# Kernel optimization log

Measured on AMD Instinct MI355X. Metric: run time of the kernel, lower is better.

Reference implementation:

```python
import jax, jax.numpy as jnp
import numpy as np

D_IN, D_OUT = 128, 128


def setup_inputs() -> dict:
    key = jax.random.key(0)
    ks = jax.random.split(key, 12)
    B = 262144
    g = 1.0 / np.sqrt(D_IN)
    gc = 1.0 / np.sqrt(D_IN + D_OUT)
    go = 1.0 / np.sqrt(D_OUT)
    return {
        "x": jax.random.normal(ks[0], (B, D_IN), jnp.float32),
        "h_prev": jax.random.normal(ks[1], (1, D_OUT), jnp.float32) * 0.1,
        "W_slow_w": jax.random.normal(ks[2], (D_OUT, D_IN), jnp.float32) * g,
        "W_slow_b": jnp.zeros((D_OUT,), jnp.float32),
        "W_fast_w": jnp.zeros((D_OUT, D_IN), jnp.float32),
        "Wi_w": jax.random.normal(ks[3], (D_OUT, D_IN), jnp.float32) * g,
        "Wi_b": jnp.zeros((D_OUT,), jnp.float32),
        "Wf_w": jax.random.normal(ks[4], (D_OUT, D_IN + D_OUT), jnp.float32) * gc,
        "Wf_b": jnp.zeros((D_OUT,), jnp.float32),
        "Wo_w": jax.random.normal(ks[5], (D_OUT, D_OUT), jnp.float32) * go,
        "Wo_b": jnp.zeros((D_OUT,), jnp.float32),
        "ln_g": jnp.ones((D_OUT,), jnp.float32),
        "ln_b": jnp.zeros((D_OUT,), jnp.float32),
    }


def _linear(x, w, b=None):
    y = x @ w.T
    return y if b is None else y + b


def _layernorm(x, g, b, eps=1e-5):
    mu = jnp.mean(x, axis=-1, keepdims=True)
    var = jnp.var(x, axis=-1, keepdims=True)
    return (x - mu) * jax.lax.rsqrt(var + eps) * g + b


def reference(x, h_prev, W_slow_w, W_slow_b, W_fast_w, Wi_w, Wi_b,
              Wf_w, Wf_b, Wo_w, Wo_b, ln_g, ln_b):
    B = x.shape[0]
    hp = jnp.broadcast_to(h_prev, (B, h_prev.shape[1]))  # [B, d_out]
    i_t = jax.nn.sigmoid(_linear(x, Wi_w, Wi_b))
    f_t = jax.nn.sigmoid(_linear(jnp.concatenate([x, hp], axis=1), Wf_w, Wf_b))
    h_slow = _linear(x, W_slow_w, W_slow_b)
    h_fast = _linear(x, W_fast_w)
    h_raw = i_t * (h_slow + h_fast) + f_t * hp
    o_t = jax.nn.sigmoid(_linear(h_raw, Wo_w, Wo_b))
    h_out = o_t * jnp.tanh(h_raw)
    return _layernorm(h_out, ln_g, ln_b)
```

## Files before the change

kernel.cpp:

```cpp
#include <hip/hip_runtime.h>
#include <hip/hip_bf16.h>
#include <hip/hip_fp16.h>


typedef __attribute__((ext_vector_type(8)))  short short8;
typedef __attribute__((ext_vector_type(16))) float f32x16;

__device__ __forceinline__ unsigned short f2bf(float f) {
    union { float f; unsigned u; } v; v.f = f;
    unsigned r = v.u + 0x7fffu + ((v.u >> 16) & 1u);
    return (unsigned short)(r >> 16);
}
__device__ __forceinline__ float bf2f(unsigned hs) {
    union { unsigned u; float f; } v; v.u = hs << 16;
    return v.f;
}
__device__ __forceinline__ unsigned pk_bf16(float lo, float hi) {
    union { __hip_bfloat162 h; unsigned u; } c;
    c.h = __float22bfloat162_rn(make_float2(lo, hi));
    return c.u;
}
__device__ __forceinline__ unsigned pk_f16(float lo, float hi) {
    union { __half2 h; unsigned u; } c;
    c.h = __floats2half2_rn(lo, hi);
    return c.u;
}
__device__ __forceinline__ float lo_f16(unsigned u) {
    union { unsigned u; __half2 h; } c; c.u = u;
    return __low2float(c.h);
}
__device__ __forceinline__ float hi_f16(unsigned u) {
    union { unsigned u; __half2 h; } c; c.u = u;
    return __high2float(c.h);
}
__device__ __forceinline__ float rcp_fast(float x) { return __builtin_amdgcn_rcpf(x); }
__device__ __forceinline__ float exp2_fast(float x) { return __builtin_amdgcn_exp2f(x); }
__device__ __forceinline__ float sigm(float x) {
    return rcp_fast(1.0f + exp2_fast(-1.4426950408889634f * x));
}
__device__ __forceinline__ float tanh_fast(float x) {
    return 1.0f - 2.0f * rcp_fast(1.0f + exp2_fast(2.8853900817779268f * x));
}
__device__ __forceinline__ f32x16 mfma_bf16(short8 a, short8 b, f32x16 c) {
    return __builtin_amdgcn_mfma_f32_32x32x16_bf16(a, b, c, 0, 0, 0);
}

#define SWZ(r) ((unsigned)(((r) & 15) << 4))

__global__ void prep_wimg(const float* __restrict__ Wi_w,
                          const float* __restrict__ Wf_w,
                          const float* __restrict__ Ws_w,
                          const float* __restrict__ Wfast_w,
                          const float* __restrict__ Wo_w,
                          unsigned short* __restrict__ Wimg) {
    int gid = blockIdx.x * 256 + threadIdx.x;
    int g = gid >> 14;
    int e = gid & 16383;
    int r = e >> 7;
    int k = (((e & 127) * 2) ^ SWZ(r)) >> 1;
    float v;
    if (g == 0)      v = Wi_w[r * 128 + k];
    else if (g == 1) v = Ws_w[r * 128 + k] + Wfast_w[r * 128 + k];
    else if (g == 2) v = Wf_w[r * 256 + k];
    else             v = Wo_w[r * 128 + k];
    Wimg[gid] = f2bf(v);
}

__global__ void prep_fbias(const float* __restrict__ Wf_w,
                           const float* __restrict__ Wf_b,
                           const float* __restrict__ hp,
                           float* __restrict__ fbias) {
    int j = threadIdx.x;
    float s = Wf_b[j];
    for (int k = 0; k < 128; ++k) s += Wf_w[j * 256 + 128 + k] * hp[k];
    fbias[j] = s;
}

__global__ __launch_bounds__(256, 2)
void cell_main(const float* __restrict__ x,
               const float* __restrict__ hp,
               const float* __restrict__ Wi_b,
               const float* __restrict__ Ws_b,
               const float* __restrict__ Wo_b,
               const float* __restrict__ ln_g,
               const float* __restrict__ ln_b,
               const unsigned short* __restrict__ Wimg,
               const float* __restrict__ fbias,
               float* __restrict__ out) {
    const int tid  = threadIdx.x;
    const int lane = tid & 63;
    const int w    = tid >> 6;
    const int lm   = lane & 31;
    const int h    = lane >> 5;

    __shared__ __align__(16) char  xh[16384];
    __shared__ __align__(16) char  wb[32768];
    __shared__ __align__(16) float prm[7 * 128];

    const size_t row0 = (size_t)blockIdx.x * 64;

    auto stageW = [&](int g) {
        const uint4* src = (const uint4*)(Wimg + (size_t)g * 16384);
        #pragma unroll
        for (int j = 0; j < 8; ++j)
            ((uint4*)wb)[j * 256 + tid] = src[j * 256 + tid];
    };
    auto WFRD = [&](int ks) -> short8 {
        const int r = w * 32 + lm;
        const unsigned off = (unsigned)(r * 256) + (((unsigned)(ks * 32 + h * 16)) ^ SWZ(r));
        return *(const short8*)(wb + off);
    };
    auto LDXF = [&](int mt, int ks) -> short8 {
        const int r = mt * 32 + lm;
        const unsigned off = (unsigned)(r * 256) + (((unsigned)(ks * 32 + h * 16)) ^ SWZ(r));
        return *(const short8*)(xh + off);
    };

    {
        const float4* xb = (const float4*)(x + row0 * 128);
        #pragma unroll
        for (int it = 0; it < 8; ++it) {
            const int idx = it * 256 + tid;
            const float4 v = xb[idx];
            const int r = idx >> 5;
            const unsigned off = ((unsigned)(r * 256 + (idx & 31) * 8)) ^ SWZ(r);
            *(uint2*)(xh + off) = make_uint2(pk_bf16(v.x, v.y), pk_bf16(v.z, v.w));
        }
        if (tid < 224) {
            const int a = tid >> 5, e4 = (tid & 31) * 4;
            float4 v;
            switch (a) {
                case 0: v = *(const float4*)(Wi_b + e4); break;
                case 1: v = *(const float4*)(Ws_b + e4); break;
                case 2: v = *(const float4*)(fbias + e4); break;
                case 3: v = *(const float4*)(hp + e4); break;
                case 4: v = *(const float4*)(Wo_b + e4); break;
                case 5: v = *(const float4*)(ln_g + e4); break;
                default: v = *(const float4*)(ln_b + e4); break;
            }
            *(float4*)(prm + a * 128 + e4) = v;
        }
        stageW(0);
    }
    __syncthreads();

    unsigned ik[16];
    {
        short8 WF[8];
        #pragma unroll
        for (int ks = 0; ks < 8; ++ks) WF[ks] = WFRD(ks);
        #pragma unroll
        for (int mt = 0; mt < 2; ++mt) {
            f32x16 acc;
            #pragma unroll
            for (int e = 0; e < 16; ++e) acc[e] = 0.f;
            #pragma unroll
            for (int ks = 0; ks < 8; ++ks)
                acc = mfma_bf16(WF[ks], LDXF(mt, ks), acc);
            #pragma unroll
            for (int q = 0; q < 4; ++q) {
                const int n0 = w * 32 + q * 8 + h * 4;
                const float4 bi = *(const float4*)(prm + 0 * 128 + n0);
                ik[mt*8+q*2+0] = pk_f16(sigm(acc[q*4+0] + bi.x), sigm(acc[q*4+1] + bi.y));
                ik[mt*8+q*2+1] = pk_f16(sigm(acc[q*4+2] + bi.z), sigm(acc[q*4+3] + bi.w));
            }
        }
    }
    __syncthreads();
    stageW(1);
    __syncthreads();

    unsigned ppk[16];
    {
        short8 WF[8];
        #pragma unroll
        for (int ks = 0; ks < 8; ++ks) WF[ks] = WFRD(ks);
        #pragma unroll
        for (int mt = 0; mt < 2; ++mt) {
            f32x16 acc;
            #pragma unroll
            for (int e = 0; e < 16; ++e) acc[e] = 0.f;
            #pragma unroll
            for (int ks = 0; ks < 8; ++ks)
                acc = mfma_bf16(WF[ks], LDXF(mt, ks), acc);
            #pragma unroll
            for (int q = 0; q < 4; ++q) {
                const int n0 = w * 32 + q * 8 + h * 4;
                const float4 bs = *(const float4*)(prm + 1 * 128 + n0);
                const unsigned ia = ik[mt*8+q*2+0], ib = ik[mt*8+q*2+1];
                ppk[mt*8+q*2+0] = pk_f16(lo_f16(ia) * (acc[q*4+0] + bs.x),
                                         hi_f16(ia) * (acc[q*4+1] + bs.y));
                ppk[mt*8+q*2+1] = pk_f16(lo_f16(ib) * (acc[q*4+2] + bs.z),
                                         hi_f16(ib) * (acc[q*4+3] + bs.w));
            }
        }
    }
    __syncthreads();
    stageW(2);
    __syncthreads();

    unsigned hpk[16];
    {
        short8 WF[8];
        #pragma unroll
        for (int ks = 0; ks < 8; ++ks) WF[ks] = WFRD(ks);
        #pragma unroll
        for (int mt = 0; mt < 2; ++mt) {
            f32x16 acc;
            #pragma unroll
            for (int e = 0; e < 16; ++e) acc[e] = 0.f;
            #pragma unroll
            for (int ks = 0; ks < 8; ++ks)
                acc = mfma_bf16(WF[ks], LDXF(mt, ks), acc);
            #pragma unroll
            for (int q = 0; q < 4; ++q) {
                const int n0 = w * 32 + q * 8 + h * 4;
                const float4 fb4 = *(const float4*)(prm + 2 * 128 + n0);
                const float4 hp4 = *(const float4*)(prm + 3 * 128 + n0);
                const unsigned pa = ppk[mt*8+q*2+0], pb = ppk[mt*8+q*2+1];
                hpk[mt*8+q*2+0] = pk_bf16(lo_f16(pa) + sigm(acc[q*4+0] + fb4.x) * hp4.x,
                                          hi_f16(pa) + sigm(acc[q*4+1] + fb4.y) * hp4.y);
                hpk[mt*8+q*2+1] = pk_bf16(lo_f16(pb) + sigm(acc[q*4+2] + fb4.z) * hp4.z,
                                          hi_f16(pb) + sigm(acc[q*4+3] + fb4.w) * hp4.w);
            }
        }
    }
    __syncthreads();

    #pragma unroll
    for (int mt = 0; mt < 2; ++mt) {
        const int r = mt * 32 + lm;
        #pragma unroll
        for (int q = 0; q < 4; ++q) {
            const unsigned off = (unsigned)(r * 256)
                + (((unsigned)((w * 32 + q * 8 + h * 4) * 2)) ^ SWZ(r));
            *(uint2*)(xh + off) = make_uint2(hpk[mt*8+q*2+0], hpk[mt*8+q*2+1]);
        }
    }
    stageW(3);
    __syncthreads();

    unsigned opk[16];
    float sums[2], ssqs[2];
    {
        short8 WF[8];
        #pragma unroll
        for (int ks = 0; ks < 8; ++ks) WF[ks] = WFRD(ks);
        #pragma unroll
        for (int mt = 0; mt < 2; ++mt) {
            f32x16 acc;
            #pragma unroll
            for (int e = 0; e < 16; ++e) acc[e] = 0.f;
            #pragma unroll
            for (int ks = 0; ks < 8; ++ks)
                acc = mfma_bf16(WF[ks], LDXF(mt, ks), acc);
            float sum = 0.f, ssq = 0.f;
            #pragma unroll
            for (int q = 0; q < 4; ++q) {
                const int n0 = w * 32 + q * 8 + h * 4;
                const float4 bo = *(const float4*)(prm + 4 * 128 + n0);
                const unsigned ha = hpk[mt*8+q*2+0], hb = hpk[mt*8+q*2+1];
                const float hv0 = sigm(acc[q*4+0] + bo.x) * tanh_fast(bf2f(ha & 0xffffu));
                const float hv1 = sigm(acc[q*4+1] + bo.y) * tanh_fast(bf2f(ha >> 16));
                const float hv2 = sigm(acc[q*4+2] + bo.z) * tanh_fast(bf2f(hb & 0xffffu));
                const float hv3 = sigm(acc[q*4+3] + bo.w) * tanh_fast(bf2f(hb >> 16));
                opk[mt*8+q*2+0] = pk_f16(hv0, hv1);
                opk[mt*8+q*2+1] = pk_f16(hv2, hv3);
                sum += hv0 + hv1 + hv2 + hv3;
                ssq += hv0*hv0 + hv1*hv1 + hv2*hv2 + hv3*hv3;
            }
            sum += __shfl_xor(sum, 32, 64);
            ssq += __shfl_xor(ssq, 32, 64);
            sums[mt] = sum; ssqs[mt] = ssq;
        }
    }
    __syncthreads();

    float* red = (float*)wb;
    if (h == 0) {
        #pragma unroll
        for (int mt = 0; mt < 2; ++mt) {
            red[((mt * 4 + w) * 32 + lm) * 2 + 0] = sums[mt];
            red[((mt * 4 + w) * 32 + lm) * 2 + 1] = ssqs[mt];
        }
    }
    __syncthreads();

    #pragma unroll
    for (int mt = 0; mt < 2; ++mt) {
        float s = 0.f, q2 = 0.f;
        #pragma unroll
        for (int ww = 0; ww < 4; ++ww) {
            s  += red[((mt * 4 + ww) * 32 + lm) * 2 + 0];
            q2 += red[((mt * 4 + ww) * 32 + lm) * 2 + 1];
        }
        const float mean = s * (1.0f / 128.0f);
        const float var  = q2 * (1.0f / 128.0f) - mean * mean;
        const float rstd = __builtin_amdgcn_rsqf(var + 1e-5f);
        float* orow = out + (row0 + (size_t)(mt * 32 + lm)) * 128;
        #pragma unroll
        for (int q = 0; q < 4; ++q) {
            const int n0 = w * 32 + q * 8 + h * 4;
            const float4 g4 = *(const float4*)(prm + 5 * 128 + n0);
            const float4 b4 = *(const float4*)(prm + 6 * 128 + n0);
            const unsigned oa = opk[mt*8+q*2+0], ob = opk[mt*8+q*2+1];
            float4 rr;
            rr.x = (lo_f16(oa) - mean) * rstd * g4.x + b4.x;
            rr.y = (hi_f16(oa) - mean) * rstd * g4.y + b4.y;
            rr.z = (lo_f16(ob) - mean) * rstd * g4.z + b4.z;
            rr.w = (hi_f16(ob) - mean) * rstd * g4.w + b4.w;
            *(float4*)(orow + n0) = rr;
        }
    }
}

extern "C" void kernel_launch(void* const* d_in, const int* in_sizes, int n_in,
                              void* d_out, int out_size, void* d_ws, size_t ws_size,
                              hipStream_t stream) {
    const float* x      = (const float*)d_in[0];
    const float* h_prev = (const float*)d_in[1];
    const float* Ws_w   = (const float*)d_in[2];
    const float* Ws_b   = (const float*)d_in[3];
    const float* Wfast  = (const float*)d_in[4];
    const float* Wi_w   = (const float*)d_in[5];
    const float* Wi_b   = (const float*)d_in[6];
    const float* Wf_w   = (const float*)d_in[7];
    const float* Wf_b   = (const float*)d_in[8];
    const float* Wo_w   = (const float*)d_in[9];
    const float* Wo_b   = (const float*)d_in[10];
    const float* ln_g   = (const float*)d_in[11];
    const float* ln_b   = (const float*)d_in[12];

    unsigned short* Wimg = (unsigned short*)d_ws;
    float*          fb   = (float*)(Wimg + 65536);

    prep_wimg<<<256, 256, 0, stream>>>(Wi_w, Wf_w, Ws_w, Wfast, Wo_w, Wimg);
    prep_fbias<<<1, 128, 0, stream>>>(Wf_w, Wf_b, h_prev, fb);

    const int B = in_sizes[0] / 128;
    const int blocks = B / 64;
    cell_main<<<blocks, 256, 0, stream>>>(x, h_prev, Wi_b, Ws_b, Wo_b,
                                          ln_g, ln_b, Wimg, fb,
                                          (float*)d_out);
}
```

Baseline: 102.5 us.

## Load MFMA weight fragments directly from global in fragment order, drop LDS weight staging

The weight prep kernel now writes each 128x128 gate matrix pre-shuffled into per-lane MFMA fragment order, so each wave reads its A operands straight from global/L2 with coalesced 16-byte loads. This removes the per-gate LDS staging buffer and the barriers around each stage, and frees LDS so more blocks can be resident. The LayerNorm output is also restaged through LDS so the final stores are fully coalesced row-contiguous float4 writes. The cost is repeated global/L2 reads of the weights in every block instead of one shared LDS copy, plus extra barriers and LDS traffic in the epilogue.

```diff
diff --git a/kernel.cpp b/kernel.cpp
--- a/kernel.cpp
+++ b/kernel.cpp
@@ -11,10 +11,6 @@
     unsigned r = v.u + 0x7fffu + ((v.u >> 16) & 1u);
     return (unsigned short)(r >> 16);
 }
-__device__ __forceinline__ float bf2f(unsigned hs) {
-    union { unsigned u; float f; } v; v.u = hs << 16;
-    return v.f;
-}
 __device__ __forceinline__ unsigned pk_bf16(float lo, float hi) {
     union { __hip_bfloat162 h; unsigned u; } c;
     c.h = __float22bfloat162_rn(make_float2(lo, hi));
@@ -33,6 +29,10 @@
     union { unsigned u; __half2 h; } c; c.u = u;
     return __high2float(c.h);
 }
+__device__ __forceinline__ float bf2f(unsigned hs) {
+    union { unsigned u; float f; } v; v.u = hs << 16;
+    return v.f;
+}
 __device__ __forceinline__ float rcp_fast(float x) { return __builtin_amdgcn_rcpf(x); }
 __device__ __forceinline__ float exp2_fast(float x) { return __builtin_amdgcn_exp2f(x); }
 __device__ __forceinline__ float sigm(float x) {
@@ -47,23 +47,26 @@
 
 #define SWZ(r) ((unsigned)(((r) & 15) << 4))
 
-__global__ void prep_wimg(const float* __restrict__ Wi_w,
-                          const float* __restrict__ Wf_w,
-                          const float* __restrict__ Ws_w,
-                          const float* __restrict__ Wfast_w,
-                          const float* __restrict__ Wo_w,
-                          unsigned short* __restrict__ Wimg) {
+__global__ void prep_weights(const float* __restrict__ Wi_w,
+                             const float* __restrict__ Wf_w,
+                             const float* __restrict__ Ws_w,
+                             const float* __restrict__ Wfast_w,
+                             const float* __restrict__ Wo_w,
+                             unsigned short* __restrict__ Wshuf) {
     int gid = blockIdx.x * 256 + threadIdx.x;
-    int g = gid >> 14;
-    int e = gid & 16383;
-    int r = e >> 7;
-    int k = (((e & 127) * 2) ^ SWZ(r)) >> 1;
+    int e    = gid & 7;
+    int lane = (gid >> 3) & 63;
+    int ks   = (gid >> 9) & 7;
+    int t    = gid >> 12;
+    int g = t >> 2, jg = t & 3;
+    int row = jg * 32 + (lane & 31);
+    int k   = ks * 16 + (lane >> 5) * 8 + e;
     float v;
-    if (g == 0)      v = Wi_w[r * 128 + k];
-    else if (g == 1) v = Ws_w[r * 128 + k] + Wfast_w[r * 128 + k];
-    else if (g == 2) v = Wf_w[r * 256 + k];
-    else             v = Wo_w[r * 128 + k];
-    Wimg[gid] = f2bf(v);
+    if (g == 0)      v = Wi_w[row * 128 + k];
+    else if (g == 1) v = Wf_w[row * 256 + k];
+    else if (g == 2) v = Ws_w[row * 128 + k] + Wfast_w[row * 128 + k];
+    else             v = Wo_w[row * 128 + k];
+    Wshuf[gid] = f2bf(v);
 }
 
 __global__ void prep_fbias(const float* __restrict__ Wf_w,
@@ -84,7 +87,7 @@
                const float* __restrict__ Wo_b,
                const float* __restrict__ ln_g,
                const float* __restrict__ ln_b,
-               const unsigned short* __restrict__ Wimg,
+               const unsigned short* __restrict__ Wshuf,
                const float* __restrict__ fbias,
                float* __restrict__ out) {
     const int tid  = threadIdx.x;
@@ -94,27 +97,11 @@
     const int h    = lane >> 5;
 
     __shared__ __align__(16) char  xh[16384];
-    __shared__ __align__(16) char  wb[32768];
     __shared__ __align__(16) float prm[7 * 128];
+    __shared__ __align__(16) float red[4][4][32][2];
+    __shared__ __align__(16) float red2[64][2];
 
     const size_t row0 = (size_t)blockIdx.x * 64;
-
-    auto stageW = [&](int g) {
-        const uint4* src = (const uint4*)(Wimg + (size_t)g * 16384);
-        #pragma unroll
-        for (int j = 0; j < 8; ++j)
-            ((uint4*)wb)[j * 256 + tid] = src[j * 256 + tid];
-    };
-    auto WFRD = [&](int ks) -> short8 {
-        const int r = w * 32 + lm;
-        const unsigned off = (unsigned)(r * 256) + (((unsigned)(ks * 32 + h * 16)) ^ SWZ(r));
-        return *(const short8*)(wb + off);
-    };
-    auto LDXF = [&](int mt, int ks) -> short8 {
-        const int r = mt * 32 + lm;
-        const unsigned off = (unsigned)(r * 256) + (((unsigned)(ks * 32 + h * 16)) ^ SWZ(r));
-        return *(const short8*)(xh + off);
-    };
 
     {
         const float4* xb = (const float4*)(x + row0 * 128);
@@ -140,15 +127,96 @@
             }
             *(float4*)(prm + a * 128 + e4) = v;
         }
-        stageW(0);
-    }
-    __syncthreads();
+    }
+    __syncthreads();
+
+    auto LDXF = [&](int mt, int ks) -> short8 {
+        const int r = mt * 32 + lm;
+        const unsigned off = (unsigned)(r * 256) + (((unsigned)(ks * 32 + h * 16)) ^ SWZ(r));
+        return *(const short8*)(xh + off);
+    };
+    const unsigned short* Wl = Wshuf + (size_t)lane * 8;
+    auto WFG = [&](int g, int ks) -> short8 {
+        return *(const short8*)(const void*)(Wl + (size_t)((g * 4 + w) * 8 + ks) * 512);
+    };
 
     unsigned ik[16];
+    #pragma unroll
+    for (int mt = 0; mt < 2; ++mt) {
+        f32x16 acc;
+        #pragma unroll
+        for (int e = 0; e < 16; ++e) acc[e] = 0.f;
+        #pragma unroll
+        for (int ks = 0; ks < 8; ++ks)
+            acc = mfma_bf16(WFG(0, ks), LDXF(mt, ks), acc);
+        #pragma unroll
+        for (int q = 0; q < 4; ++q) {
+            const int n0 = w * 32 + q * 8 + h * 4;
+            const float4 bi = *(const float4*)(prm + 0 * 128 + n0);
+            ik[mt*8+q*2+0] = pk_f16(sigm(acc[q*4+0] + bi.x), sigm(acc[q*4+1] + bi.y));
+            ik[mt*8+q*2+1] = pk_f16(sigm(acc[q*4+2] + bi.z), sigm(acc[q*4+3] + bi.w));
+        }
+    }
+
+    unsigned ppk[16];
+    #pragma unroll
+    for (int mt = 0; mt < 2; ++mt) {
+        f32x16 acc;
+        #pragma unroll
+        for (int e = 0; e < 16; ++e) acc[e] = 0.f;
+        #pragma unroll
+        for (int ks = 0; ks < 8; ++ks)
+            acc = mfma_bf16(WFG(2, ks), LDXF(mt, ks), acc);
+        #pragma unroll
+        for (int q = 0; q < 4; ++q) {
+            const int n0 = w * 32 + q * 8 + h * 4;
+            const float4 bs = *(const float4*)(prm + 1 * 128 + n0);
+            const unsigned ia = ik[mt*8+q*2+0], ib = ik[mt*8+q*2+1];
+            ppk[mt*8+q*2+0] = pk_f16(lo_f16(ia) * (acc[q*4+0] + bs.x),
+                                     hi_f16(ia) * (acc[q*4+1] + bs.y));
+            ppk[mt*8+q*2+1] = pk_f16(lo_f16(ib) * (acc[q*4+2] + bs.z),
+                                     hi_f16(ib) * (acc[q*4+3] + bs.w));
+        }
+    }
+
+    unsigned hpk[16];
+    #pragma unroll
+    for (int mt = 0; mt < 2; ++mt) {
+        f32x16 acc;
+        #pragma unroll
+        for (int e = 0; e < 16; ++e) acc[e] = 0.f;
+        #pragma unroll
+        for (int ks = 0; ks < 8; ++ks)
+            acc = mfma_bf16(WFG(1, ks), LDXF(mt, ks), acc);
+        #pragma unroll
+        for (int q = 0; q < 4; ++q) {
+            const int n0 = w * 32 + q * 8 + h * 4;
+            const float4 fb4 = *(const float4*)(prm + 2 * 128 + n0);
+            const float4 hp4 = *(const float4*)(prm + 3 * 128 + n0);
+            const unsigned pa = ppk[mt*8+q*2+0], pb = ppk[mt*8+q*2+1];
+            hpk[mt*8+q*2+0] = pk_bf16(lo_f16(pa) + sigm(acc[q*4+0] + fb4.x) * hp4.x,
+                                      hi_f16(pa) + sigm(acc[q*4+1] + fb4.y) * hp4.y);
+            hpk[mt*8+q*2+1] = pk_bf16(lo_f16(pb) + sigm(acc[q*4+2] + fb4.z) * hp4.z,
+                                      hi_f16(pb) + sigm(acc[q*4+3] + fb4.w) * hp4.w);
+        }
+    }
+    __syncthreads();
+
+    #pragma unroll
+    for (int mt = 0; mt < 2; ++mt) {
+        const int r = mt * 32 + lm;
+        #pragma unroll
+        for (int q = 0; q < 4; ++q) {
+            const unsigned off = (unsigned)(r * 256)
+                + (((unsigned)((w * 32 + q * 8 + h * 4) * 2)) ^ SWZ(r));
+            *(uint2*)(xh + off) = make_uint2(hpk[mt*8+q*2+0], hpk[mt*8+q*2+1]);
+        }
+    }
+    __syncthreads();
+
+    unsigned opk[16];
     {
-        short8 WF[8];
-        #pragma unroll
-        for (int ks = 0; ks < 8; ++ks) WF[ks] = WFRD(ks);
+        float sums[2], ssqs[2];
         #pragma unroll
         for (int mt = 0; mt < 2; ++mt) {
             f32x16 acc;
@@ -156,104 +224,7 @@
             for (int e = 0; e < 16; ++e) acc[e] = 0.f;
             #pragma unroll
             for (int ks = 0; ks < 8; ++ks)
-                acc = mfma_bf16(WF[ks], LDXF(mt, ks), acc);
-            #pragma unroll
-            for (int q = 0; q < 4; ++q) {
-                const int n0 = w * 32 + q * 8 + h * 4;
-                const float4 bi = *(const float4*)(prm + 0 * 128 + n0);
-                ik[mt*8+q*2+0] = pk_f16(sigm(acc[q*4+0] + bi.x), sigm(acc[q*4+1] + bi.y));
-                ik[mt*8+q*2+1] = pk_f16(sigm(acc[q*4+2] + bi.z), sigm(acc[q*4+3] + bi.w));
-            }
-        }
-    }
-    __syncthreads();
-    stageW(1);
-    __syncthreads();
-
-    unsigned ppk[16];
-    {
-        short8 WF[8];
-        #pragma unroll
-        for (int ks = 0; ks < 8; ++ks) WF[ks] = WFRD(ks);
-        #pragma unroll
-        for (int mt = 0; mt < 2; ++mt) {
-            f32x16 acc;
-            #pragma unroll
-            for (int e = 0; e < 16; ++e) acc[e] = 0.f;
-            #pragma unroll
-            for (int ks = 0; ks < 8; ++ks)
-                acc = mfma_bf16(WF[ks], LDXF(mt, ks), acc);
-            #pragma unroll
-            for (int q = 0; q < 4; ++q) {
-                const int n0 = w * 32 + q * 8 + h * 4;
-                const float4 bs = *(const float4*)(prm + 1 * 128 + n0);
-                const unsigned ia = ik[mt*8+q*2+0], ib = ik[mt*8+q*2+1];
-                ppk[mt*8+q*2+0] = pk_f16(lo_f16(ia) * (acc[q*4+0] + bs.x),
-                                         hi_f16(ia) * (acc[q*4+1] + bs.y));
-                ppk[mt*8+q*2+1] = pk_f16(lo_f16(ib) * (acc[q*4+2] + bs.z),
-                                         hi_f16(ib) * (acc[q*4+3] + bs.w));
-            }
-        }
-    }
-    __syncthreads();
-    stageW(2);
-    __syncthreads();
-
-    unsigned hpk[16];
-    {
-        short8 WF[8];
-        #pragma unroll
-        for (int ks = 0; ks < 8; ++ks) WF[ks] = WFRD(ks);
-        #pragma unroll
-        for (int mt = 0; mt < 2; ++mt) {
-            f32x16 acc;
-            #pragma unroll
-            for (int e = 0; e < 16; ++e) acc[e] = 0.f;
-            #pragma unroll
-            for (int ks = 0; ks < 8; ++ks)
-                acc = mfma_bf16(WF[ks], LDXF(mt, ks), acc);
-            #pragma unroll
-            for (int q = 0; q < 4; ++q) {
-                const int n0 = w * 32 + q * 8 + h * 4;
-                const float4 fb4 = *(const float4*)(prm + 2 * 128 + n0);
-                const float4 hp4 = *(const float4*)(prm + 3 * 128 + n0);
-                const unsigned pa = ppk[mt*8+q*2+0], pb = ppk[mt*8+q*2+1];
-                hpk[mt*8+q*2+0] = pk_bf16(lo_f16(pa) + sigm(acc[q*4+0] + fb4.x) * hp4.x,
-                                          hi_f16(pa) + sigm(acc[q*4+1] + fb4.y) * hp4.y);
-                hpk[mt*8+q*2+1] = pk_bf16(lo_f16(pb) + sigm(acc[q*4+2] + fb4.z) * hp4.z,
-                                          hi_f16(pb) + sigm(acc[q*4+3] + fb4.w) * hp4.w);
-            }
-        }
-    }
-    __syncthreads();
-
-    #pragma unroll
-    for (int mt = 0; mt < 2; ++mt) {
-        const int r = mt * 32 + lm;
-        #pragma unroll
-        for (int q = 0; q < 4; ++q) {
-            const unsigned off = (unsigned)(r * 256)
-                + (((unsigned)((w * 32 + q * 8 + h * 4) * 2)) ^ SWZ(r));
-            *(uint2*)(xh + off) = make_uint2(hpk[mt*8+q*2+0], hpk[mt*8+q*2+1]);
-        }
-    }
-    stageW(3);
-    __syncthreads();
-
-    unsigned opk[16];
-    float sums[2], ssqs[2];
-    {
-        short8 WF[8];
-        #pragma unroll
-        for (int ks = 0; ks < 8; ++ks) WF[ks] = WFRD(ks);
-        #pragma unroll
-        for (int mt = 0; mt < 2; ++mt) {
-            f32x16 acc;
-            #pragma unroll
-            for (int e = 0; e < 16; ++e) acc[e] = 0.f;
-            #pragma unroll
-            for (int ks = 0; ks < 8; ++ks)
-                acc = mfma_bf16(WF[ks], LDXF(mt, ks), acc);
+                acc = mfma_bf16(WFG(3, ks), LDXF(mt, ks), acc);
             float sum = 0.f, ssq = 0.f;
             #pragma unroll
             for (int q = 0; q < 4; ++q) {
@@ -273,44 +244,58 @@
             ssq += __shfl_xor(ssq, 32, 64);
             sums[mt] = sum; ssqs[mt] = ssq;
         }
-    }
-    __syncthreads();
-
-    float* red = (float*)wb;
-    if (h == 0) {
-        #pragma unroll
-        for (int mt = 0; mt < 2; ++mt) {
-            red[((mt * 4 + w) * 32 + lm) * 2 + 0] = sums[mt];
-            red[((mt * 4 + w) * 32 + lm) * 2 + 1] = ssqs[mt];
-        }
-    }
-    __syncthreads();
-
-    #pragma unroll
-    for (int mt = 0; mt < 2; ++mt) {
+        if (h == 0) {
+            #pragma unroll
+            for (int mt = 0; mt < 2; ++mt) {
+                red[mt][w][lm][0] = sums[mt];
+                red[mt][w][lm][1] = ssqs[mt];
+            }
+        }
+    }
+    __syncthreads();
+
+    #pragma unroll
+    for (int mt = 0; mt < 2; ++mt) {
+        const int r = mt * 32 + lm;
+        #pragma unroll
+        for (int q = 0; q < 4; ++q) {
+            const unsigned off = (unsigned)(r * 256)
+                + (((unsigned)((w * 32 + q * 8 + h * 4) * 2)) ^ SWZ(r));
+            *(uint2*)(xh + off) = make_uint2(opk[mt*8+q*2+0], opk[mt*8+q*2+1]);
+        }
+    }
+    if (tid < 64) {
+        const int mt = tid >> 5, l = tid & 31;
         float s = 0.f, q2 = 0.f;
         #pragma unroll
         for (int ww = 0; ww < 4; ++ww) {
-            s  += red[((mt * 4 + ww) * 32 + lm) * 2 + 0];
-            q2 += red[((mt * 4 + ww) * 32 + lm) * 2 + 1];
+            s  += red[mt][ww][l][0];
+            q2 += red[mt][ww][l][1];
         }
         const float mean = s * (1.0f / 128.0f);
         const float var  = q2 * (1.0f / 128.0f) - mean * mean;
-        const float rstd = __builtin_amdgcn_rsqf(var + 1e-5f);
-        float* orow = out + (row0 + (size_t)(mt * 32 + lm)) * 128;
-        #pragma unroll
-        for (int q = 0; q < 4; ++q) {
-            const int n0 = w * 32 + q * 8 + h * 4;
-            const float4 g4 = *(const float4*)(prm + 5 * 128 + n0);
-            const float4 b4 = *(const float4*)(prm + 6 * 128 + n0);
-            const unsigned oa = opk[mt*8+q*2+0], ob = opk[mt*8+q*2+1];
-            float4 rr;
-            rr.x = (lo_f16(oa) - mean) * rstd * g4.x + b4.x;
-            rr.y = (hi_f16(oa) - mean) * rstd * g4.y + b4.y;
-            rr.z = (lo_f16(ob) - mean) * rstd * g4.z + b4.z;
-            rr.w = (hi_f16(ob) - mean) * rstd * g4.w + b4.w;
-            *(float4*)(orow + n0) = rr;
-        }
+        red2[tid][0] = mean;
+        red2[tid][1] = __builtin_amdgcn_rsqf(var + 1e-5f);
+    }
+    __syncthreads();
+
+    float* ob = out + row0 * 128;
+    #pragma unroll
+    for (int it = 0; it < 8; ++it) {
+        const int idx = it * 256 + tid;
+        const int r = idx >> 5;
+        const int c4 = (idx & 31) * 4;
+        const unsigned off = (unsigned)(r * 256) + (((unsigned)(c4 * 2)) ^ SWZ(r));
+        const uint2 hv = *(const uint2*)(xh + off);
+        const float mean = red2[r][0], rstd = red2[r][1];
+        const float4 g4 = *(const float4*)(prm + 5 * 128 + c4);
+        const float4 b4 = *(const float4*)(prm + 6 * 128 + c4);
+        float4 rr;
+        rr.x = (lo_f16(hv.x) - mean) * rstd * g4.x + b4.x;
+        rr.y = (hi_f16(hv.x) - mean) * rstd * g4.y + b4.y;
+        rr.z = (lo_f16(hv.y) - mean) * rstd * g4.z + b4.z;
+        rr.w = (hi_f16(hv.y) - mean) * rstd * g4.w + b4.w;
+        *(float4*)(ob + (size_t)idx * 4) = rr;
     }
 }
 
@@ -331,15 +316,15 @@
     const float* ln_g   = (const float*)d_in[11];
     const float* ln_b   = (const float*)d_in[12];
 
-    unsigned short* Wimg = (unsigned short*)d_ws;
-    float*          fb   = (float*)(Wimg + 65536);
-
-    prep_wimg<<<256, 256, 0, stream>>>(Wi_w, Wf_w, Ws_w, Wfast, Wo_w, Wimg);
+    unsigned short* Wshuf = (unsigned short*)d_ws;
+    float*          fb    = (float*)(Wshuf + 65536);
+
+    prep_weights<<<256, 256, 0, stream>>>(Wi_w, Wf_w, Ws_w, Wfast, Wo_w, Wshuf);
     prep_fbias<<<1, 128, 0, stream>>>(Wf_w, Wf_b, h_prev, fb);
 
     const int B = in_sizes[0] / 128;
     const int blocks = B / 64;
     cell_main<<<blocks, 256, 0, stream>>>(x, h_prev, Wi_b, Ws_b, Wo_b,
-                                          ln_g, ln_b, Wimg, fb,
+                                          ln_g, ln_b, Wshuf, fb,
                                           (float*)d_out);
 }
```

New measurement: 92.47 us. -9.7%, faster.
